# Kernel optimization log

Hardware: AMD Instinct MI355X
Metric: run time of the kernel (lower is better)

The kernel has to match this reference:

```python
import jax, jax.numpy as jnp
import numpy as np

B, T, C, H, Wimg = 16, 6, 4, 420, 312
PH, PW = 14, 12
E = 768
GH, GW = H // PH, Wimg // PW  # 30, 26 -> 780 patches
N_VALID = 390


def setup_inputs() -> dict:
    key = jax.random.key(0)
    kx, kw, kb = jax.random.split(key, 3)
    x = jax.random.normal(kx, (B, T, C, H, Wimg), dtype=jnp.float32)
    W = jax.random.normal(kw, (E, C, PH, PW), dtype=jnp.float32) * 0.02
    b = jax.random.normal(kb, (E,), dtype=jnp.float32) * 0.02
    # static patch mask: keep half the patches (unique, sorted indices like torch.nonzero)
    rng = np.random.default_rng(0)
    valid = np.sort(rng.choice(GH * GW, size=N_VALID, replace=False)).astype(np.int32)
    return {"x": x, "W": W, "b": b, "valid_indices": jnp.asarray(valid)}


def reference(x, W, b, valid_indices):
    Bv, Tv, Cv, Hv, Wv = x.shape
    Ev, _, ph, pw = W.shape
    gh, gw = Hv // ph, Wv // pw
    # non-overlapping stride=kernel conv == patchify + GEMM
    xp = x.reshape(Bv * Tv, Cv, gh, ph, gw, pw)
    out = jnp.einsum('ncipjq,ecpq->nije', xp, W) + b  # [B*T, gh, gw, E]
    out = out.reshape(Bv, Tv, gh * gw, Ev)            # [B, T, n_patches, E]
    return out[:, :, valid_indices, :]                # [B, T, n_valid, E]
```

## Files before the change

kernel.cpp:

```cpp
#include <hip/hip_runtime.h>

#define M_TOT 37440
#define N_E   768
#define K_TOT 672
#define NV    390
#define GWID  26
#define PHh   14
#define PWw   12
#define IMW   312
#define CSTRIDE 131040
#define NSTRIDE 524160

#define NKT   7
#define TPAD  104
#define ROWT  728

typedef short bf16x8 __attribute__((ext_vector_type(8)));
typedef float f32x4  __attribute__((ext_vector_type(4)));
typedef unsigned short u16;
typedef u16 u16x4 __attribute__((ext_vector_type(4)));

#define A_PAD_BYTES 54512640u
#define W_PAD_BYTES 1118208u
#define WS_NEEDED   (A_PAD_BYTES + W_PAD_BYTES)

#define NBLK_A 8190
#define NBLK_W 168

#define NWG   1758
#define SWZ_Q 219
#define SWZ_R 6

static __device__ __forceinline__ u16 f2bf(float f) {
  unsigned u = __builtin_bit_cast(unsigned, f);
  u = (u + 0x7FFFu + ((u >> 16) & 1u)) >> 16;
  return (u16)u;
}

#define GLOAD_LDS16(g, l) \
  __builtin_amdgcn_global_load_lds((const __attribute__((address_space(1))) void*)(g), \
                                   (__attribute__((address_space(3))) void*)(l), 16, 0, 0)

__global__ __launch_bounds__(256) void patchify(
    const float* __restrict__ x, const float* __restrict__ w,
    const int* __restrict__ valid, u16* __restrict__ Ap, u16* __restrict__ Wp) {
  const int bid = blockIdx.x;
  const int tid = threadIdx.x;
  if (bid < NBLK_A) {
    const int g  = bid * 256 + tid;
    const int m  = g / 56;
    const int rr = g - m * 56;
    const int t  = rr >> 3, run = rr & 7;
    const int nimg = m / NV;
    const int v    = m - nimg * NV;
    const int gidx = valid[v];
    const int gi = gidx / GWID, gj = gidx - gi * GWID;
    const int c  = rr / PHh,    p  = rr - c * PHh;
    const float* src = x + (size_t)nimg * NSTRIDE + (size_t)c * CSTRIDE
                         + (size_t)(gi * PHh + p) * IMW + gj * PWw;
    f32x4 f0 = *(const f32x4*)(src + 0);
    f32x4 f1 = *(const f32x4*)(src + 4);
    f32x4 f2 = *(const f32x4*)(src + 8);
    u16* dst = Ap + (size_t)m * ROWT + t * TPAD + run * 12;
    u16x4 h0 = {f2bf(f0.x), f2bf(f0.y), f2bf(f0.z), f2bf(f0.w)};
    u16x4 h1 = {f2bf(f1.x), f2bf(f1.y), f2bf(f1.z), f2bf(f1.w)};
    u16x4 h2 = {f2bf(f2.x), f2bf(f2.y), f2bf(f2.z), f2bf(f2.w)};
    *(u16x4*)(dst + 0) = h0;
    *(u16x4*)(dst + 4) = h1;
    *(u16x4*)(dst + 8) = h2;
  } else {
    const int g  = (bid - NBLK_A) * 256 + tid;
    const int n  = g / 56;
    const int rr = g - n * 56;
    const int t  = rr >> 3, run = rr & 7;
    const float* src = w + (size_t)n * K_TOT + rr * 12;
    f32x4 f0 = *(const f32x4*)(src + 0);
    f32x4 f1 = *(const f32x4*)(src + 4);
    f32x4 f2 = *(const f32x4*)(src + 8);
    u16* dst = Wp + (size_t)n * ROWT + t * TPAD + run * 12;
    u16x4 h0 = {f2bf(f0.x), f2bf(f0.y), f2bf(f0.z), f2bf(f0.w)};
    u16x4 h1 = {f2bf(f1.x), f2bf(f1.y), f2bf(f1.z), f2bf(f1.w)};
    u16x4 h2 = {f2bf(f2.x), f2bf(f2.y), f2bf(f2.z), f2bf(f2.w)};
    *(u16x4*)(dst + 0) = h0;
    *(u16x4*)(dst + 4) = h1;
    *(u16x4*)(dst + 8) = h2;
  }
}

__global__ __launch_bounds__(256, 3) void gemm_bf16(
    const u16* __restrict__ Ap, const u16* __restrict__ Wp,
    const float* __restrict__ bias, float* __restrict__ out) {
  __shared__ u16 lds[2][128 * TPAD];

  const int tid  = threadIdx.x;
  const int lane = tid & 63;
  const int wid  = tid >> 6;
  const int wr   = wid >> 1, wc = wid & 1;
  const int lrow = lane & 15, lhi = lane >> 4;

  const int orig = blockIdx.x;
  const int xcd = orig & 7, pos = orig >> 3;
  const int lid = (xcd < SWZ_R ? xcd * (SWZ_Q + 1)
                               : SWZ_R * (SWZ_Q + 1) + (xcd - SWZ_R) * SWZ_Q) + pos;
  const int n0 = (lid % 6) * 128;
  const int m0 = (lid / 6) * 128;

  int goff[13];
  const u16* gbase;
  if (wid < 2) {
    #pragma unroll
    for (int j = 0; j < 13; ++j) {
      const int g = (wid * 13 + j) * 64 + lane;
      const int row = g / 13, col = g - row * 13;
      int ar = m0 + row; if (ar > M_TOT - 1) ar = M_TOT - 1;
      goff[j] = ar * ROWT + col * 8;
    }
    gbase = Ap;
  } else {
    #pragma unroll
    for (int j = 0; j < 13; ++j) {
      const int g = ((wid - 2) * 13 + j) * 64 + lane;
      const int row = g / 13, col = g - row * 13;
      goff[j] = (n0 + row) * ROWT + col * 8;
    }
    gbase = Wp;
  }
  char* ldst = (char*)&lds[wid >> 1][0] + (wid & 1) * (13 * 1024);

  f32x4 acc[4][4];
  #pragma unroll
  for (int i = 0; i < 4; ++i)
    #pragma unroll
    for (int j = 0; j < 4; ++j)
      acc[i][j] = (f32x4){0.f, 0.f, 0.f, 0.f};

  for (int t = 0; t < NKT; ++t) {
    #pragma unroll
    for (int j = 0; j < 13; ++j)
      GLOAD_LDS16(gbase + goff[j] + t * TPAD, ldst + j * 1024);
    __syncthreads();

    #pragma unroll
    for (int kk = 0; kk < 3; ++kk) {
      bf16x8 a[4], bfr[4];
      #pragma unroll
      for (int i = 0; i < 4; ++i)
        a[i] = *(const bf16x8*)&lds[0][(wr * 64 + i * 16 + lrow) * TPAD + kk * 32 + lhi * 8];
      #pragma unroll
      for (int j = 0; j < 4; ++j)
        bfr[j] = *(const bf16x8*)&lds[1][(wc * 64 + j * 16 + lrow) * TPAD + kk * 32 + lhi * 8];
      #pragma unroll
      for (int i = 0; i < 4; ++i)
        #pragma unroll
        for (int j = 0; j < 4; ++j)
          acc[i][j] = __builtin_amdgcn_mfma_f32_16x16x32_bf16(a[i], bfr[j], acc[i][j], 0, 0, 0);
    }
    __syncthreads();
  }

  float bv[4];
  #pragma unroll
  for (int j = 0; j < 4; ++j)
    bv[j] = bias[n0 + wc * 64 + j * 16 + lrow];

  #pragma unroll
  for (int i = 0; i < 4; ++i) {
    const int mbase = m0 + wr * 64 + i * 16 + lhi * 4;
    #pragma unroll
    for (int j = 0; j < 4; ++j) {
      const int e = n0 + wc * 64 + j * 16 + lrow;
      float* op = out + (size_t)mbase * N_E + e;
      #pragma unroll
      for (int tt = 0; tt < 4; ++tt) {
        if (mbase + tt < M_TOT) op[(size_t)tt * N_E] = acc[i][j][tt] + bv[j];
      }
    }
  }
}

#define ROWB 104
__global__ __launch_bounds__(256) void patch_gemm_fused(
    const float* __restrict__ x, const float* __restrict__ w,
    const float* __restrict__ bias, const int* __restrict__ valid,
    float* __restrict__ out) {
  __shared__ u16 Alds[128 * ROWB];
  __shared__ u16 Blds[128 * ROWB];
  const int tid  = threadIdx.x;
  const int lane = tid & 63;
  const int wid  = tid >> 6;
  const int wr   = wid >> 1, wc = wid & 1;
  const int lrow = lane & 15, lhi = lane >> 4;
  const int m0 = blockIdx.x * 128;
  const int n0 = blockIdx.y * 128;
  const int arow = tid & 127;
  int m = m0 + arow;
  if (m >= M_TOT) m = M_TOT - 1;
  const int nimg = m / NV;
  const int v    = m - nimg * NV;
  const int g    = valid[v];
  const int gi   = g / GWID;
  const int gj   = g - gi * GWID;
  const float* xrow = x + (size_t)nimg * NSTRIDE + (size_t)(gi * PHh) * IMW + gj * PWw;
  const int half = tid >> 7;
  const float* wrow = w + (size_t)(n0 + arow) * K_TOT;
  f32x4 acc[4][4];
  #pragma unroll
  for (int i = 0; i < 4; ++i)
    #pragma unroll
    for (int j = 0; j < 4; ++j)
      acc[i][j] = (f32x4){0.f, 0.f, 0.f, 0.f};
  for (int t = 0; t < 7; ++t) {
    #pragma unroll
    for (int it = 0; it < 4; ++it) {
      const int run = half + it * 2;
      const int rr  = t * 8 + run;
      const int c   = rr / PHh;
      const int p   = rr - c * PHh;
      const float* src = xrow + (size_t)c * CSTRIDE + p * IMW;
      f32x4 f0 = *(const f32x4*)(src + 0);
      f32x4 f1 = *(const f32x4*)(src + 4);
      f32x4 f2 = *(const f32x4*)(src + 8);
      u16x4 h0 = {f2bf(f0.x), f2bf(f0.y), f2bf(f0.z), f2bf(f0.w)};
      u16x4 h1 = {f2bf(f1.x), f2bf(f1.y), f2bf(f1.z), f2bf(f1.w)};
      u16x4 h2 = {f2bf(f2.x), f2bf(f2.y), f2bf(f2.z), f2bf(f2.w)};
      u16* dst = &Alds[arow * ROWB + run * 12];
      *(u16x4*)(dst + 0) = h0;
      *(u16x4*)(dst + 4) = h1;
      *(u16x4*)(dst + 8) = h2;
    }
    #pragma unroll
    for (int i = 0; i < 6; ++i) {
      const int col = half * 48 + i * 8;
      const float* src = wrow + t * 96 + col;
      f32x4 f0 = *(const f32x4*)(src + 0);
      f32x4 f1 = *(const f32x4*)(src + 4);
      u16x4 h0 = {f2bf(f0.x), f2bf(f0.y), f2bf(f0.z), f2bf(f0.w)};
      u16x4 h1 = {f2bf(f1.x), f2bf(f1.y), f2bf(f1.z), f2bf(f1.w)};
      u16* dst = &Blds[arow * ROWB + col];
      *(u16x4*)(dst + 0) = h0;
      *(u16x4*)(dst + 4) = h1;
    }
    __syncthreads();
    #pragma unroll
    for (int kk = 0; kk < 3; ++kk) {
      bf16x8 a[4], b[4];
      #pragma unroll
      for (int i = 0; i < 4; ++i)
        a[i] = *(const bf16x8*)&Alds[(wr * 64 + i * 16 + lrow) * ROWB + kk * 32 + lhi * 8];
      #pragma unroll
      for (int j = 0; j < 4; ++j)
        b[j] = *(const bf16x8*)&Blds[(wc * 64 + j * 16 + lrow) * ROWB + kk * 32 + lhi * 8];
      #pragma unroll
      for (int i = 0; i < 4; ++i)
        #pragma unroll
        for (int j = 0; j < 4; ++j)
          acc[i][j] = __builtin_amdgcn_mfma_f32_16x16x32_bf16(a[i], b[j], acc[i][j], 0, 0, 0);
    }
    __syncthreads();
  }
  float bv[4];
  #pragma unroll
  for (int j = 0; j < 4; ++j)
    bv[j] = bias[n0 + wc * 64 + j * 16 + lrow];
  #pragma unroll
  for (int i = 0; i < 4; ++i) {
    const int mbase = m0 + wr * 64 + i * 16 + lhi * 4;
    #pragma unroll
    for (int j = 0; j < 4; ++j) {
      const int e = n0 + wc * 64 + j * 16 + lrow;
      float* op = out + (size_t)mbase * N_E + e;
      #pragma unroll
      for (int tt = 0; tt < 4; ++tt) {
        if (mbase + tt < M_TOT) op[(size_t)tt * N_E] = acc[i][j][tt] + bv[j];
      }
    }
  }
}

extern "C" void kernel_launch(void* const* d_in, const int* in_sizes, int n_in,
                              void* d_out, int out_size, void* d_ws, size_t ws_size,
                              hipStream_t stream) {
  const float* x     = (const float*)d_in[0];
  const float* w     = (const float*)d_in[1];
  const float* b     = (const float*)d_in[2];
  const int*   valid = (const int*)d_in[3];
  float* out = (float*)d_out;

  if (ws_size >= (size_t)WS_NEEDED) {
    u16* Aws = (u16*)d_ws;
    u16* Wws = (u16*)((char*)d_ws + A_PAD_BYTES);
    patchify<<<NBLK_A + NBLK_W, 256, 0, stream>>>(x, w, valid, Aws, Wws);
    gemm_bf16<<<NWG, 256, 0, stream>>>(Aws, Wws, b, out);
  } else {
    dim3 grid((M_TOT + 127) / 128, N_E / 128);
    patch_gemm_fused<<<grid, dim3(256), 0, stream>>>(x, w, b, valid, out);
  }
}
```

Baseline: 384.8 us.

## Enlarge GEMM tile to 256x128 with 8 waves and vectorized output stores

The bf16 GEMM moves from 128x128 tiles with 4 waves to 256x128 tiles with 8 waves per workgroup. This halves the workgroup count and lets each loaded W tile be reused across twice as many rows. The MFMA operands are swapped so each lane holds four consecutive output columns, which allows 16-byte float4 stores and float4 bias loads in place of scalar strided stores. LDS per block grows to about 78 KB, which may reduce how many workgroups fit on each CU.

```diff
diff --git a/kernel.cpp b/kernel.cpp
--- a/kernel.cpp
+++ b/kernel.cpp
@@ -27,9 +27,9 @@
 #define NBLK_A 8190
 #define NBLK_W 168
 
-#define NWG   1758
-#define SWZ_Q 219
-#define SWZ_R 6
+#define NWG   882
+#define SWZ_Q 110
+#define SWZ_R 2
 
 static __device__ __forceinline__ u16 f2bf(float f) {
   unsigned u = __builtin_bit_cast(unsigned, f);
@@ -87,15 +87,18 @@
   }
 }
 
-__global__ __launch_bounds__(256, 3) void gemm_bf16(
+__global__ __launch_bounds__(512, 4) void gemm_bf16(
     const u16* __restrict__ Ap, const u16* __restrict__ Wp,
     const float* __restrict__ bias, float* __restrict__ out) {
-  __shared__ u16 lds[2][128 * TPAD];
+  __shared__ u16 lds[384 * TPAD];
+  u16* Awlds = &lds[0];
+  u16* Wwlds = &lds[256 * TPAD];
 
   const int tid  = threadIdx.x;
   const int lane = tid & 63;
   const int wid  = tid >> 6;
-  const int wr   = wid >> 1, wc = wid & 1;
+  const int wr   = wid >> 1;
+  const int wc   = wid & 1;
   const int lrow = lane & 15, lhi = lane >> 4;
 
   const int orig = blockIdx.x;
@@ -103,29 +106,25 @@
   const int lid = (xcd < SWZ_R ? xcd * (SWZ_Q + 1)
                                : SWZ_R * (SWZ_Q + 1) + (xcd - SWZ_R) * SWZ_Q) + pos;
   const int n0 = (lid % 6) * 128;
-  const int m0 = (lid / 6) * 128;
-
-  int goff[13];
-  const u16* gbase;
-  if (wid < 2) {
-    #pragma unroll
-    for (int j = 0; j < 13; ++j) {
-      const int g = (wid * 13 + j) * 64 + lane;
-      const int row = g / 13, col = g - row * 13;
+  const int m0 = (lid / 6) * 256;
+
+  int goff[10];
+  #pragma unroll
+  for (int j = 0; j < 10; ++j) {
+    const int c = j * 8 + wid;
+    if (c < 52) {
+      const int idx = c * 64 + lane;
+      const int row = idx / 13, col = idx - row * 13;
       int ar = m0 + row; if (ar > M_TOT - 1) ar = M_TOT - 1;
       goff[j] = ar * ROWT + col * 8;
-    }
-    gbase = Ap;
-  } else {
-    #pragma unroll
-    for (int j = 0; j < 13; ++j) {
-      const int g = ((wid - 2) * 13 + j) * 64 + lane;
-      const int row = g / 13, col = g - row * 13;
+    } else if (c < 78) {
+      const int idx = (c - 52) * 64 + lane;
+      const int row = idx / 13, col = idx - row * 13;
       goff[j] = (n0 + row) * ROWT + col * 8;
-    }
-    gbase = Wp;
-  }
-  char* ldst = (char*)&lds[wid >> 1][0] + (wid & 1) * (13 * 1024);
+    } else {
+      goff[j] = 0;
+    }
+  }
 
   f32x4 acc[4][4];
   #pragma unroll
@@ -136,8 +135,14 @@
 
   for (int t = 0; t < NKT; ++t) {
     #pragma unroll
-    for (int j = 0; j < 13; ++j)
-      GLOAD_LDS16(gbase + goff[j] + t * TPAD, ldst + j * 1024);
+    for (int j = 0; j < 10; ++j) {
+      const int c = j * 8 + wid;
+      if (c < 52) {
+        GLOAD_LDS16(Ap + goff[j] + t * TPAD, (char*)Awlds + c * 1024);
+      } else if (c < 78) {
+        GLOAD_LDS16(Wp + goff[j] + t * TPAD, (char*)Wwlds + (c - 52) * 1024);
+      }
+    }
     __syncthreads();
 
     #pragma unroll
@@ -145,34 +150,33 @@
       bf16x8 a[4], bfr[4];
       #pragma unroll
       for (int i = 0; i < 4; ++i)
-        a[i] = *(const bf16x8*)&lds[0][(wr * 64 + i * 16 + lrow) * TPAD + kk * 32 + lhi * 8];
+        a[i] = *(const bf16x8*)&Awlds[(wr * 64 + i * 16 + lrow) * TPAD + kk * 32 + lhi * 8];
       #pragma unroll
       for (int j = 0; j < 4; ++j)
-        bfr[j] = *(const bf16x8*)&lds[1][(wc * 64 + j * 16 + lrow) * TPAD + kk * 32 + lhi * 8];
+        bfr[j] = *(const bf16x8*)&Wwlds[(wc * 64 + j * 16 + lrow) * TPAD + kk * 32 + lhi * 8];
       #pragma unroll
       for (int i = 0; i < 4; ++i)
         #pragma unroll
         for (int j = 0; j < 4; ++j)
-          acc[i][j] = __builtin_amdgcn_mfma_f32_16x16x32_bf16(a[i], bfr[j], acc[i][j], 0, 0, 0);
+          acc[i][j] = __builtin_amdgcn_mfma_f32_16x16x32_bf16(bfr[j], a[i], acc[i][j], 0, 0, 0);
     }
     __syncthreads();
   }
 
-  float bv[4];
+  f32x4 bv[4];
   #pragma unroll
   for (int j = 0; j < 4; ++j)
-    bv[j] = bias[n0 + wc * 64 + j * 16 + lrow];
+    bv[j] = *(const f32x4*)&bias[n0 + wc * 64 + j * 16 + lhi * 4];
 
   #pragma unroll
   for (int i = 0; i < 4; ++i) {
-    const int mbase = m0 + wr * 64 + i * 16 + lhi * 4;
-    #pragma unroll
-    for (int j = 0; j < 4; ++j) {
-      const int e = n0 + wc * 64 + j * 16 + lrow;
-      float* op = out + (size_t)mbase * N_E + e;
-      #pragma unroll
-      for (int tt = 0; tt < 4; ++tt) {
-        if (mbase + tt < M_TOT) op[(size_t)tt * N_E] = acc[i][j][tt] + bv[j];
+    const int m = m0 + wr * 64 + i * 16 + lrow;
+    if (m < M_TOT) {
+      float* orow = out + (size_t)m * N_E + n0 + wc * 64 + lhi * 4;
+      #pragma unroll
+      for (int j = 0; j < 4; ++j) {
+        f32x4 v = acc[i][j] + bv[j];
+        *(f32x4*)(orow + j * 16) = v;
       }
     }
   }
@@ -290,7 +294,7 @@
     u16* Aws = (u16*)d_ws;
     u16* Wws = (u16*)((char*)d_ws + A_PAD_BYTES);
     patchify<<<NBLK_A + NBLK_W, 256, 0, stream>>>(x, w, valid, Aws, Wws);
-    gemm_bf16<<<NWG, 256, 0, stream>>>(Aws, Wws, b, out);
+    gemm_bf16<<<NWG, 512, 0, stream>>>(Aws, Wws, b, out);
   } else {
     dim3 grid((M_TOT + 127) / 128, N_E / 128);
     patch_gemm_fused<<<grid, dim3(256), 0, stream>>>(x, w, b, valid, out);
```

Result: faster. 376.8 us (-2.1%).
